# Optimization experiments

Measured on AMD Instinct MI355X. Metric: run time of the kernel, lower is better.

Reference implementation:

```python
import jax, jax.numpy as jnp
import numpy as np

NUM_HEADS = 8
LN_EPS = 1e-5


def setup_inputs() -> dict:
    key = jax.random.key(0)
    k1, k2, k3 = jax.random.split(key, 3)
    B, N, C = 1, 4096, 256
    before = jax.random.normal(k1, (B, N, C), dtype=jnp.float32)
    after = jax.random.normal(k2, (B, N, C), dtype=jnp.float32)
    W_qkv = jax.random.normal(k3, (3 * C, C), dtype=jnp.float32) * (C ** -0.5)
    d = C // NUM_HEADS
    gamma = jnp.ones((d,), dtype=jnp.float32)
    beta = jnp.zeros((d,), dtype=jnp.float32)
    return {"before": before, "after": after, "W_qkv": W_qkv, "gamma": gamma, "beta": beta}


def _qkv_norm(x, W_qkv, gamma, beta, H):
    # x: [B,N,C] -> q,k,v each [B,H,N,d], LayerNorm over d applied to all of qkv
    B, N, C = x.shape
    d = C // H
    t = jnp.einsum('bnc,oc->bno', x, W_qkv)            # [B,N,3C]
    t = t.reshape(B, N, 3, H, d).transpose(2, 0, 3, 1, 4)  # [3,B,H,N,d]
    mu = jnp.mean(t, axis=-1, keepdims=True)
    var = jnp.mean(jnp.square(t - mu), axis=-1, keepdims=True)
    t = (t - mu) * jax.lax.rsqrt(var + LN_EPS) * gamma + beta
    return t[0], t[1], t[2]


def _cross_attn(q, k, v, scale):
    # q,k,v: [B,H,N,d] -> context [B,N,C]
    attn = jax.nn.softmax(jnp.einsum('bhqd,bhkd->bhqk', q, k) * scale, axis=-1)
    ctx = jnp.einsum('bhqk,bhkd->bhqd', attn, v)
    B, H, N, d = ctx.shape
    return ctx.transpose(0, 2, 1, 3).reshape(B, N, H * d)


def reference(before, after, W_qkv, gamma, beta):
    H = NUM_HEADS
    C = before.shape[-1]
    d = C // H
    scale = d ** -0.5
    q_b, k_b, v_b = _qkv_norm(before, W_qkv, gamma, beta, H)
    q_a, k_a, v_a = _qkv_norm(after, W_qkv, gamma, beta, H)
    context_a = _cross_attn(q_b, k_a, v_a, scale)  # before attends to after
    context_b = _cross_attn(q_a, k_b, v_b, scale)  # after attends to before
    return (context_b, context_a)
```

## Files before the change

### kernel.cpp

```cpp
#include <hip/hip_runtime.h>


typedef __attribute__((ext_vector_type(8))) short short8;
typedef __attribute__((ext_vector_type(4))) float float4v;
typedef __attribute__((ext_vector_type(4))) unsigned int uint4v;

#define NTOK 4096
#define CDIM 256
#define HEADS 8
#define DHEAD 32

#define QOFF 0
#define KOFF (2*HEADS*NTOK*DHEAD)
#define VOFF (2*(2*HEADS*NTOK*DHEAD))
#define WOFF (3*(2*HEADS*NTOK*DHEAD))

__device__ inline unsigned short f2bf(float f) {
    union { float f; unsigned u; } v; v.f = f;
    unsigned r = v.u + 0x7FFFu + ((v.u >> 16) & 1u);
    return (unsigned short)(r >> 16);
}

__global__ __launch_bounds__(256) void wconv_kernel(
    const float* __restrict__ W, unsigned short* __restrict__ ws)
{
    int idx = blockIdx.x*256 + threadIdx.x;
    int R = idx >> 5, oct = idx & 31;
    int C = oct * 8;
    const float4* p = reinterpret_cast<const float4*>(W + R*CDIM + C);
    float4 a = p[0], b = p[1];
    short8 f;
    f[0]=(short)f2bf(a.x); f[1]=(short)f2bf(a.y); f[2]=(short)f2bf(a.z); f[3]=(short)f2bf(a.w);
    f[4]=(short)f2bf(b.x); f[5]=(short)f2bf(b.y); f[6]=(short)f2bf(b.z); f[7]=(short)f2bf(b.w);
    int o32 = R >> 5, r = R & 31;
    int kk = C >> 5, quad = (C >> 3) & 3;
    int dst = o32*8192 + (kk*2 + (r>>4))*512 + (quad*16 + (r&15))*8;
    *reinterpret_cast<short8*>(ws + WOFF + dst) = f;
}

__global__ __launch_bounds__(256) void qkv_ln_kernel(
    const float* __restrict__ before, const float* __restrict__ after,
    const float* __restrict__ gamma, const float* __restrict__ beta,
    unsigned short* __restrict__ ws)
{
    const int tid  = threadIdx.x;
    const int lane = tid & 63;
    const int w    = tid >> 6;
    const int quad = lane >> 4;
    const int l16  = lane & 15;
    const int rt   = blockIdx.x >> 3;
    const int oq   = blockIdx.x & 7;

    const int mrow_frag = rt*64 + w*16 + l16;
    const int inp_f = mrow_frag >> 12;
    const int n_f   = mrow_frag & 4095;
    const float* x = inp_f ? after : before;

    short8 afrag[8];
#pragma unroll
    for (int kk = 0; kk < 8; kk++) {
        const float4* p = reinterpret_cast<const float4*>(x + n_f*CDIM + kk*32 + quad*8);
        float4 a = p[0], b = p[1];
        short8 f;
        f[0]=(short)f2bf(a.x); f[1]=(short)f2bf(a.y); f[2]=(short)f2bf(a.z); f[3]=(short)f2bf(a.w);
        f[4]=(short)f2bf(b.x); f[5]=(short)f2bf(b.y); f[6]=(short)f2bf(b.z); f[7]=(short)f2bf(b.w);
        afrag[kk] = f;
    }

    const float g0  = gamma[l16], g1  = gamma[16+l16];
    const float be0 = beta[l16],  be1 = beta[16+l16];
    const float cscale = 0.17677669529663687f * 1.4426950408889634f;

    const int mrow_out  = rt*64 + w*16 + quad*4;
    const int inp_o     = mrow_out >> 12;
    const int n_o_base  = mrow_out & 4095;

    const unsigned short* wbf = ws + WOFF;

    for (int o32 = oq*3; o32 < oq*3 + 3; o32++) {
        const unsigned short* wb = wbf + o32*8192 + lane*8;
        float4v acc0 = {0.f,0.f,0.f,0.f}, acc1 = {0.f,0.f,0.f,0.f};
#pragma unroll
        for (int kk = 0; kk < 8; kk++) {
            short8 b0 = *reinterpret_cast<const short8*>(wb + (kk*2    )*512);
            short8 b1 = *reinterpret_cast<const short8*>(wb + (kk*2 + 1)*512);
            acc0 = __builtin_amdgcn_mfma_f32_16x16x32_bf16(afrag[kk], b0, acc0, 0,0,0);
            acc1 = __builtin_amdgcn_mfma_f32_16x16x32_bf16(afrag[kk], b1, acc1, 0,0,0);
        }

        const int which = o32 >> 3;
        const int h     = o32 & 7;
        unsigned short* qk = ws + (which == 0 ? QOFF : KOFF) + ((inp_o*HEADS + h)*NTOK)*DHEAD;
        unsigned short* vt = ws + VOFF + ((inp_o*HEADS + h)*DHEAD)*NTOK;
        const float qs = (which == 0) ? cscale : 1.0f;

#pragma unroll
        for (int i = 0; i < 4; i++) {
            float sum = acc0[i] + acc1[i];
            float sq  = acc0[i]*acc0[i] + acc1[i]*acc1[i];
#pragma unroll
            for (int m = 1; m < 16; m <<= 1) {
                sum += __shfl_xor(sum, m);
                sq  += __shfl_xor(sq,  m);
            }
            float mu   = sum * (1.0f/32.0f);
            float var  = sq * (1.0f/32.0f) - mu*mu;
            float rstd = rsqrtf(var + 1e-5f);
            float v0 = ((acc0[i]-mu)*rstd*g0 + be0) * qs;
            float v1 = ((acc1[i]-mu)*rstd*g1 + be1) * qs;
            int n = n_o_base + i;
            if (which < 2) {
                qk[n*DHEAD + l16]      = f2bf(v0);
                qk[n*DHEAD + 16 + l16] = f2bf(v1);
            } else {
                int kb = n >> 5, ki = n & 31;
                int slot = ((ki & 15) >> 2)*8 + (ki & 3) + ((ki >> 4) << 2);
                int kp2 = kb*32 + slot;
                vt[l16*NTOK + kp2]       = f2bf(v0);
                vt[(16+l16)*NTOK + kp2]  = f2bf(v1);
            }
        }
    }
}

__global__ __launch_bounds__(256, 4) void attn_kernel(
    const unsigned short* __restrict__ ws, float* __restrict__ out)
{
    __shared__ unsigned short vlds[2][32*136];

    const int b    = blockIdx.x;
    const int xcd  = b & 7;
    const int i_   = b >> 3;
    const int combo = xcd*2 + (i_ >> 6);
    const int h  = combo & 7;
    const int X  = combo >> 3;
    const int qb = i_ & 63;

    const int qinp = 1 - X, kvinp = X;
    const int tid  = threadIdx.x;
    const int lane = tid & 63;
    const int w    = tid >> 6;
    const int qh   = w & 1;
    const int kh   = w >> 1;
    const int quad = lane >> 4;
    const int l16  = lane & 15;

    const unsigned short* qbase = ws + QOFF + ((qinp*HEADS + h)*NTOK)*DHEAD;
    const unsigned short* kbase = ws + KOFF + ((kvinp*HEADS + h)*NTOK)*DHEAD;
    const unsigned short* vbase = ws + VOFF + ((kvinp*HEADS + h)*DHEAD)*NTOK;

    const int q0 = qb*64 + qh*32;
    const short8 qf0 = *reinterpret_cast<const short8*>(qbase + (q0 + l16)*DHEAD      + quad*8);
    const short8 qf1 = *reinterpret_cast<const short8*>(qbase + (q0 + 16 + l16)*DHEAD + quad*8);

    const unsigned short* kp   = kbase + (kh*2048 + l16)*DHEAD + quad*8;
    const unsigned short* vsrc = vbase + kh*2048;

    const short8 ones = {0x3F80,0x3F80,0x3F80,0x3F80,0x3F80,0x3F80,0x3F80,0x3F80};

    float4v O00 = {0,0,0,0}, O01 = {0,0,0,0}, O10 = {0,0,0,0}, O11 = {0,0,0,0};
    float4v L0  = {0,0,0,0}, L1  = {0,0,0,0};

    unsigned short* vh = vlds[kh];
    const int t2 = qh*64 + lane;

    for (int j = 0; j < 16; j++) {
        __syncthreads();
#pragma unroll
        for (int r = 0; r < 4; r++) {
            int c = t2 + 128*r;
            short8 d = *reinterpret_cast<const short8*>(vsrc + (c>>4)*NTOK + j*128 + (c&15)*8);
            *reinterpret_cast<short8*>(vh + (c>>4)*136 + (c&15)*8) = d;
        }
        __syncthreads();

#pragma unroll
        for (int grp = 0; grp < 4; grp++) {
            short8 kf0 = *reinterpret_cast<const short8*>(kp + (j*128 + grp*32     )*DHEAD);
            short8 kf1 = *reinterpret_cast<const short8*>(kp + (j*128 + grp*32 + 16)*DHEAD);
            short8 v0  = *reinterpret_cast<const short8*>(vh + l16*136      + grp*32 + quad*8);
            short8 v1  = *reinterpret_cast<const short8*>(vh + (16+l16)*136 + grp*32 + quad*8);
#pragma unroll
            for (int s = 0; s < 2; s++) {
                const short8 qf = s ? qf1 : qf0;
                float4v z = {0,0,0,0};
                float4v S0 = __builtin_amdgcn_mfma_f32_16x16x32_bf16(kf0, qf, z, 0,0,0);
                float4v S1 = __builtin_amdgcn_mfma_f32_16x16x32_bf16(kf1, qf, z, 0,0,0);
                union { float f; unsigned u; } u0,u1,u2,u3,u4,u5,u6,u7;
                u0.f = __builtin_amdgcn_exp2f(S0[0]);
                u1.f = __builtin_amdgcn_exp2f(S0[1]);
                u2.f = __builtin_amdgcn_exp2f(S0[2]);
                u3.f = __builtin_amdgcn_exp2f(S0[3]);
                u4.f = __builtin_amdgcn_exp2f(S1[0]);
                u5.f = __builtin_amdgcn_exp2f(S1[1]);
                u6.f = __builtin_amdgcn_exp2f(S1[2]);
                u7.f = __builtin_amdgcn_exp2f(S1[3]);
                union { short8 s8; uint4v u4v; } pf;
                pf.u4v[0] = __builtin_amdgcn_perm(u1.u, u0.u, 0x07060302u);
                pf.u4v[1] = __builtin_amdgcn_perm(u3.u, u2.u, 0x07060302u);
                pf.u4v[2] = __builtin_amdgcn_perm(u5.u, u4.u, 0x07060302u);
                pf.u4v[3] = __builtin_amdgcn_perm(u7.u, u6.u, 0x07060302u);
                if (s == 0) {
                    O00 = __builtin_amdgcn_mfma_f32_16x16x32_bf16(pf.s8, v0,   O00, 0,0,0);
                    O01 = __builtin_amdgcn_mfma_f32_16x16x32_bf16(pf.s8, v1,   O01, 0,0,0);
                    L0  = __builtin_amdgcn_mfma_f32_16x16x32_bf16(pf.s8, ones, L0,  0,0,0);
                } else {
                    O10 = __builtin_amdgcn_mfma_f32_16x16x32_bf16(pf.s8, v0,   O10, 0,0,0);
                    O11 = __builtin_amdgcn_mfma_f32_16x16x32_bf16(pf.s8, v1,   O11, 0,0,0);
                    L1  = __builtin_amdgcn_mfma_f32_16x16x32_bf16(pf.s8, ones, L1,  0,0,0);
                }
            }
        }
    }

    __syncthreads();

    float* comb = reinterpret_cast<float*>(&vlds[0][0]) + qh*(32*34);
    if (kh == 1) {
#pragma unroll
        for (int s = 0; s < 2; s++)
#pragma unroll
            for (int i = 0; i < 4; i++) {
                int row = s*16 + quad*4 + i;
                comb[row*34 + l16]      = (s ? O10[i] : O00[i]);
                comb[row*34 + 16 + l16] = (s ? O11[i] : O01[i]);
                if (l16 == 0) comb[row*34 + 32] = (s ? L1[i] : L0[i]);
            }
    }
    __syncthreads();

    if (kh == 0) {
        float* ob = out + (size_t)X*NTOK*CDIM + h*DHEAD;
#pragma unroll
        for (int s = 0; s < 2; s++) {
#pragma unroll
            for (int i = 0; i < 4; i++) {
                int row = s*16 + quad*4 + i;
                float l = (s ? L1[i] : L0[i]) + comb[row*34 + 32];
                float inv = 1.0f / l;
                float a = ((s ? O10[i] : O00[i]) + comb[row*34 + l16])      * inv;
                float b = ((s ? O11[i] : O01[i]) + comb[row*34 + 16 + l16]) * inv;
                int orow = q0 + row;
                ob[orow*CDIM + l16]      = a;
                ob[orow*CDIM + 16 + l16] = b;
            }
        }
    }
}

extern "C" void kernel_launch(void* const* d_in, const int* in_sizes, int n_in,
                              void* d_out, int out_size, void* d_ws, size_t ws_size,
                              hipStream_t stream)
{
    const float* before = (const float*)d_in[0];
    const float* after  = (const float*)d_in[1];
    const float* W      = (const float*)d_in[2];
    const float* gamma  = (const float*)d_in[3];
    const float* beta   = (const float*)d_in[4];
    float* out          = (float*)d_out;
    unsigned short* ws  = (unsigned short*)d_ws;

    hipLaunchKernelGGL(wconv_kernel, dim3(96), dim3(256), 0, stream, W, ws);
    hipLaunchKernelGGL(qkv_ln_kernel, dim3(1024), dim3(256), 0, stream,
                       before, after, gamma, beta, ws);
    hipLaunchKernelGGL(attn_kernel, dim3(1024), dim3(256), 0, stream, ws, out);
}
```

Before: 146.5 us.

## Double-buffer V tiles in LDS with register prefetch and hoist K loads

V tiles now go through two LDS buffers. The next tile's global loads are issued into registers before the current tile's MFMA work and written to the other buffer afterwards, so one barrier per iteration replaces two. All four groups of K fragments are also loaded up front to overlap their latency with compute. This doubles the LDS footprint, which may lower occupancy, and the extra prefetch and K registers add register pressure.

Result: no change. 145.1 us (-0.9%).

```diff
diff --git a/kernel.cpp b/kernel.cpp
--- a/kernel.cpp
+++ b/kernel.cpp
@@ -126,7 +126,7 @@
 __global__ __launch_bounds__(256, 4) void attn_kernel(
     const unsigned short* __restrict__ ws, float* __restrict__ out)
 {
-    __shared__ unsigned short vlds[2][32*136];
+    __shared__ unsigned short vlds[2][2][32*136];
 
     const int b    = blockIdx.x;
     const int xcd  = b & 7;
@@ -161,31 +161,49 @@
     float4v O00 = {0,0,0,0}, O01 = {0,0,0,0}, O10 = {0,0,0,0}, O11 = {0,0,0,0};
     float4v L0  = {0,0,0,0}, L1  = {0,0,0,0};
 
-    unsigned short* vh = vlds[kh];
     const int t2 = qh*64 + lane;
+    const int vr = t2 >> 4;
+    const int vc = (t2 & 15)*8;
+
+    {
+        short8 vreg[4];
+#pragma unroll
+        for (int r = 0; r < 4; r++)
+            vreg[r] = *reinterpret_cast<const short8*>(vsrc + (vr + 8*r)*NTOK + vc);
+#pragma unroll
+        for (int r = 0; r < 4; r++)
+            *reinterpret_cast<short8*>(&vlds[kh][0][(vr + 8*r)*136 + vc]) = vreg[r];
+    }
 
     for (int j = 0; j < 16; j++) {
         __syncthreads();
-#pragma unroll
-        for (int r = 0; r < 4; r++) {
-            int c = t2 + 128*r;
-            short8 d = *reinterpret_cast<const short8*>(vsrc + (c>>4)*NTOK + j*128 + (c&15)*8);
-            *reinterpret_cast<short8*>(vh + (c>>4)*136 + (c&15)*8) = d;
-        }
-        __syncthreads();
-
+        const unsigned short* vh = vlds[kh][j&1];
+
+        short8 vreg[4];
+        const bool pf = (j + 1 < 16);
+        if (pf) {
+#pragma unroll
+            for (int r = 0; r < 4; r++)
+                vreg[r] = *reinterpret_cast<const short8*>(vsrc + (vr + 8*r)*NTOK + (j+1)*128 + vc);
+        }
+
+        short8 kf0[4], kf1[4];
 #pragma unroll
         for (int grp = 0; grp < 4; grp++) {
-            short8 kf0 = *reinterpret_cast<const short8*>(kp + (j*128 + grp*32     )*DHEAD);
-            short8 kf1 = *reinterpret_cast<const short8*>(kp + (j*128 + grp*32 + 16)*DHEAD);
-            short8 v0  = *reinterpret_cast<const short8*>(vh + l16*136      + grp*32 + quad*8);
-            short8 v1  = *reinterpret_cast<const short8*>(vh + (16+l16)*136 + grp*32 + quad*8);
+            kf0[grp] = *reinterpret_cast<const short8*>(kp + (j*128 + grp*32     )*DHEAD);
+            kf1[grp] = *reinterpret_cast<const short8*>(kp + (j*128 + grp*32 + 16)*DHEAD);
+        }
+
+#pragma unroll
+        for (int grp = 0; grp < 4; grp++) {
+            short8 v0 = *reinterpret_cast<const short8*>(vh + l16*136      + grp*32 + quad*8);
+            short8 v1 = *reinterpret_cast<const short8*>(vh + (16+l16)*136 + grp*32 + quad*8);
 #pragma unroll
             for (int s = 0; s < 2; s++) {
                 const short8 qf = s ? qf1 : qf0;
                 float4v z = {0,0,0,0};
-                float4v S0 = __builtin_amdgcn_mfma_f32_16x16x32_bf16(kf0, qf, z, 0,0,0);
-                float4v S1 = __builtin_amdgcn_mfma_f32_16x16x32_bf16(kf1, qf, z, 0,0,0);
+                float4v S0 = __builtin_amdgcn_mfma_f32_16x16x32_bf16(kf0[grp], qf, z, 0,0,0);
+                float4v S1 = __builtin_amdgcn_mfma_f32_16x16x32_bf16(kf1[grp], qf, z, 0,0,0);
                 union { float f; unsigned u; } u0,u1,u2,u3,u4,u5,u6,u7;
                 u0.f = __builtin_amdgcn_exp2f(S0[0]);
                 u1.f = __builtin_amdgcn_exp2f(S0[1]);
@@ -195,27 +213,33 @@
                 u5.f = __builtin_amdgcn_exp2f(S1[1]);
                 u6.f = __builtin_amdgcn_exp2f(S1[2]);
                 u7.f = __builtin_amdgcn_exp2f(S1[3]);
-                union { short8 s8; uint4v u4v; } pf;
-                pf.u4v[0] = __builtin_amdgcn_perm(u1.u, u0.u, 0x07060302u);
-                pf.u4v[1] = __builtin_amdgcn_perm(u3.u, u2.u, 0x07060302u);
-                pf.u4v[2] = __builtin_amdgcn_perm(u5.u, u4.u, 0x07060302u);
-                pf.u4v[3] = __builtin_amdgcn_perm(u7.u, u6.u, 0x07060302u);
+                union { short8 s8; uint4v u4v; } pfr;
+                pfr.u4v[0] = __builtin_amdgcn_perm(u1.u, u0.u, 0x07060302u);
+                pfr.u4v[1] = __builtin_amdgcn_perm(u3.u, u2.u, 0x07060302u);
+                pfr.u4v[2] = __builtin_amdgcn_perm(u5.u, u4.u, 0x07060302u);
+                pfr.u4v[3] = __builtin_amdgcn_perm(u7.u, u6.u, 0x07060302u);
                 if (s == 0) {
-                    O00 = __builtin_amdgcn_mfma_f32_16x16x32_bf16(pf.s8, v0,   O00, 0,0,0);
-                    O01 = __builtin_amdgcn_mfma_f32_16x16x32_bf16(pf.s8, v1,   O01, 0,0,0);
-                    L0  = __builtin_amdgcn_mfma_f32_16x16x32_bf16(pf.s8, ones, L0,  0,0,0);
+                    O00 = __builtin_amdgcn_mfma_f32_16x16x32_bf16(pfr.s8, v0,   O00, 0,0,0);
+                    O01 = __builtin_amdgcn_mfma_f32_16x16x32_bf16(pfr.s8, v1,   O01, 0,0,0);
+                    L0  = __builtin_amdgcn_mfma_f32_16x16x32_bf16(pfr.s8, ones, L0,  0,0,0);
                 } else {
-                    O10 = __builtin_amdgcn_mfma_f32_16x16x32_bf16(pf.s8, v0,   O10, 0,0,0);
-                    O11 = __builtin_amdgcn_mfma_f32_16x16x32_bf16(pf.s8, v1,   O11, 0,0,0);
-                    L1  = __builtin_amdgcn_mfma_f32_16x16x32_bf16(pf.s8, ones, L1,  0,0,0);
+                    O10 = __builtin_amdgcn_mfma_f32_16x16x32_bf16(pfr.s8, v0,   O10, 0,0,0);
+                    O11 = __builtin_amdgcn_mfma_f32_16x16x32_bf16(pfr.s8, v1,   O11, 0,0,0);
+                    L1  = __builtin_amdgcn_mfma_f32_16x16x32_bf16(pfr.s8, ones, L1,  0,0,0);
                 }
             }
         }
+
+        if (pf) {
+#pragma unroll
+            for (int r = 0; r < 4; r++)
+                *reinterpret_cast<short8*>(&vlds[kh][(j+1)&1][(vr + 8*r)*136 + vc]) = vreg[r];
+        }
     }
 
     __syncthreads();
 
-    float* comb = reinterpret_cast<float*>(&vlds[0][0]) + qh*(32*34);
+    float* comb = reinterpret_cast<float*>(&vlds[0][0][0]) + qh*(32*34);
     if (kh == 1) {
 #pragma unroll
         for (int s = 0; s < 2; s++)
```

## Split attention key range across two blocks with atomic accumulation and normalize pass

Applied to the files above, without the earlier changes.

Doubles the attention grid so each block handles half of the keys (a split-K style scheme). Partial unnormalized outputs and row sums are accumulated with atomicAdd into the zeroed output and a workspace buffer, and a new kernel then divides by the row sum. The aim is more parallelism and occupancy, at the cost of two memsets, float atomics, an extra launch and a full extra pass over the output. Softmax still has no max subtraction, as before.

Result: slower. 155.4 us (+6.1%).

```diff
diff --git a/kernel.cpp b/kernel.cpp
--- a/kernel.cpp
+++ b/kernel.cpp
@@ -14,6 +14,7 @@
 #define KOFF (2*HEADS*NTOK*DHEAD)
 #define VOFF (2*(2*HEADS*NTOK*DHEAD))
 #define WOFF (3*(2*HEADS*NTOK*DHEAD))
+#define LOFF (WOFF + 24*8192)
 
 __device__ inline unsigned short f2bf(float f) {
     union { float f; unsigned u; } v; v.f = f;
@@ -131,17 +132,18 @@
     const int b    = blockIdx.x;
     const int xcd  = b & 7;
     const int i_   = b >> 3;
-    const int combo = xcd*2 + (i_ >> 6);
-    const int h  = combo & 7;
-    const int X  = combo >> 3;
-    const int qb = i_ & 63;
+    const int combo = xcd*2 + (i_ >> 7);
+    const int h   = combo & 7;
+    const int X   = combo >> 3;
+    const int qb  = (i_ >> 1) & 63;
+    const int khо = i_ & 1;
 
     const int qinp = 1 - X, kvinp = X;
     const int tid  = threadIdx.x;
     const int lane = tid & 63;
     const int w    = tid >> 6;
     const int qh   = w & 1;
-    const int kh   = w >> 1;
+    const int khi  = w >> 1;
     const int quad = lane >> 4;
     const int l16  = lane & 15;
 
@@ -150,27 +152,29 @@
     const unsigned short* vbase = ws + VOFF + ((kvinp*HEADS + h)*DHEAD)*NTOK;
 
     const int q0 = qb*64 + qh*32;
+    const int k0 = khо*2048 + khi*1024;
     const short8 qf0 = *reinterpret_cast<const short8*>(qbase + (q0 + l16)*DHEAD      + quad*8);
     const short8 qf1 = *reinterpret_cast<const short8*>(qbase + (q0 + 16 + l16)*DHEAD + quad*8);
 
-    const unsigned short* kp   = kbase + (kh*2048 + l16)*DHEAD + quad*8;
-    const unsigned short* vsrc = vbase + kh*2048;
+    const unsigned short* kp   = kbase + (k0 + l16)*DHEAD + quad*8;
+    const unsigned short* vsrc = vbase + k0;
 
     const short8 ones = {0x3F80,0x3F80,0x3F80,0x3F80,0x3F80,0x3F80,0x3F80,0x3F80};
 
     float4v O00 = {0,0,0,0}, O01 = {0,0,0,0}, O10 = {0,0,0,0}, O11 = {0,0,0,0};
     float4v L0  = {0,0,0,0}, L1  = {0,0,0,0};
 
-    unsigned short* vh = vlds[kh];
+    unsigned short* vh = vlds[khi];
     const int t2 = qh*64 + lane;
-
-    for (int j = 0; j < 16; j++) {
+    const int vr = t2 >> 4;
+    const int vc = (t2 & 15)*8;
+
+    for (int j = 0; j < 8; j++) {
         __syncthreads();
 #pragma unroll
         for (int r = 0; r < 4; r++) {
-            int c = t2 + 128*r;
-            short8 d = *reinterpret_cast<const short8*>(vsrc + (c>>4)*NTOK + j*128 + (c&15)*8);
-            *reinterpret_cast<short8*>(vh + (c>>4)*136 + (c&15)*8) = d;
+            short8 d = *reinterpret_cast<const short8*>(vsrc + (vr + 8*r)*NTOK + j*128 + vc);
+            *reinterpret_cast<short8*>(vh + (vr + 8*r)*136 + vc) = d;
         }
         __syncthreads();
 
@@ -195,19 +199,19 @@
                 u5.f = __builtin_amdgcn_exp2f(S1[1]);
                 u6.f = __builtin_amdgcn_exp2f(S1[2]);
                 u7.f = __builtin_amdgcn_exp2f(S1[3]);
-                union { short8 s8; uint4v u4v; } pf;
-                pf.u4v[0] = __builtin_amdgcn_perm(u1.u, u0.u, 0x07060302u);
-                pf.u4v[1] = __builtin_amdgcn_perm(u3.u, u2.u, 0x07060302u);
-                pf.u4v[2] = __builtin_amdgcn_perm(u5.u, u4.u, 0x07060302u);
-                pf.u4v[3] = __builtin_amdgcn_perm(u7.u, u6.u, 0x07060302u);
+                union { short8 s8; uint4v u4v; } pfr;
+                pfr.u4v[0] = __builtin_amdgcn_perm(u1.u, u0.u, 0x07060302u);
+                pfr.u4v[1] = __builtin_amdgcn_perm(u3.u, u2.u, 0x07060302u);
+                pfr.u4v[2] = __builtin_amdgcn_perm(u5.u, u4.u, 0x07060302u);
+                pfr.u4v[3] = __builtin_amdgcn_perm(u7.u, u6.u, 0x07060302u);
                 if (s == 0) {
-                    O00 = __builtin_amdgcn_mfma_f32_16x16x32_bf16(pf.s8, v0,   O00, 0,0,0);
-                    O01 = __builtin_amdgcn_mfma_f32_16x16x32_bf16(pf.s8, v1,   O01, 0,0,0);
-                    L0  = __builtin_amdgcn_mfma_f32_16x16x32_bf16(pf.s8, ones, L0,  0,0,0);
+                    O00 = __builtin_amdgcn_mfma_f32_16x16x32_bf16(pfr.s8, v0,   O00, 0,0,0);
+                    O01 = __builtin_amdgcn_mfma_f32_16x16x32_bf16(pfr.s8, v1,   O01, 0,0,0);
+                    L0  = __builtin_amdgcn_mfma_f32_16x16x32_bf16(pfr.s8, ones, L0,  0,0,0);
                 } else {
-                    O10 = __builtin_amdgcn_mfma_f32_16x16x32_bf16(pf.s8, v0,   O10, 0,0,0);
-                    O11 = __builtin_amdgcn_mfma_f32_16x16x32_bf16(pf.s8, v1,   O11, 0,0,0);
-                    L1  = __builtin_amdgcn_mfma_f32_16x16x32_bf16(pf.s8, ones, L1,  0,0,0);
+                    O10 = __builtin_amdgcn_mfma_f32_16x16x32_bf16(pfr.s8, v0,   O10, 0,0,0);
+                    O11 = __builtin_amdgcn_mfma_f32_16x16x32_bf16(pfr.s8, v1,   O11, 0,0,0);
+                    L1  = __builtin_amdgcn_mfma_f32_16x16x32_bf16(pfr.s8, ones, L1,  0,0,0);
                 }
             }
         }
@@ -216,7 +220,7 @@
     __syncthreads();
 
     float* comb = reinterpret_cast<float*>(&vlds[0][0]) + qh*(32*34);
-    if (kh == 1) {
+    if (khi == 1) {
 #pragma unroll
         for (int s = 0; s < 2; s++)
 #pragma unroll
@@ -229,23 +233,42 @@
     }
     __syncthreads();
 
-    if (kh == 0) {
+    if (khi == 0) {
         float* ob = out + (size_t)X*NTOK*CDIM + h*DHEAD;
+        float* lp = reinterpret_cast<float*>(const_cast<unsigned short*>(ws) + LOFF)
+                    + (X*HEADS + h)*NTOK;
 #pragma unroll
         for (int s = 0; s < 2; s++) {
 #pragma unroll
             for (int i = 0; i < 4; i++) {
                 int row = s*16 + quad*4 + i;
                 float l = (s ? L1[i] : L0[i]) + comb[row*34 + 32];
-                float inv = 1.0f / l;
-                float a = ((s ? O10[i] : O00[i]) + comb[row*34 + l16])      * inv;
-                float b = ((s ? O11[i] : O01[i]) + comb[row*34 + 16 + l16]) * inv;
+                float a = (s ? O10[i] : O00[i]) + comb[row*34 + l16];
+                float bb = (s ? O11[i] : O01[i]) + comb[row*34 + 16 + l16];
                 int orow = q0 + row;
-                ob[orow*CDIM + l16]      = a;
-                ob[orow*CDIM + 16 + l16] = b;
-            }
-        }
-    }
+                atomicAdd(&ob[orow*CDIM + l16],      a);
+                atomicAdd(&ob[orow*CDIM + 16 + l16], bb);
+                if (l16 == 0) atomicAdd(&lp[orow], l);
+            }
+        }
+    }
+}
+
+__global__ __launch_bounds__(256) void norm_kernel(
+    float* __restrict__ out, const unsigned short* __restrict__ ws)
+{
+    const float* l = reinterpret_cast<const float*>(ws + LOFF);
+    int idx = blockIdx.x*256 + threadIdx.x;
+    int o = idx * 4;
+    int c = o & 255;
+    int n = (o >> 8) & 4095;
+    int X = o >> 20;
+    float lv = l[(X*HEADS + (c >> 5))*NTOK + n];
+    float inv = 1.0f / lv;
+    float4* p = reinterpret_cast<float4*>(out) + idx;
+    float4 v = *p;
+    v.x *= inv; v.y *= inv; v.z *= inv; v.w *= inv;
+    *p = v;
 }
 
 extern "C" void kernel_launch(void* const* d_in, const int* in_sizes, int n_in,
@@ -260,8 +283,12 @@
     float* out          = (float*)d_out;
     unsigned short* ws  = (unsigned short*)d_ws;
 
+    hipMemsetAsync(d_out, 0, (size_t)out_size * sizeof(float), stream);
+    hipMemsetAsync(ws + LOFF, 0, (size_t)2*HEADS*NTOK*sizeof(float), stream);
+
     hipLaunchKernelGGL(wconv_kernel, dim3(96), dim3(256), 0, stream, W, ws);
     hipLaunchKernelGGL(qkv_ln_kernel, dim3(1024), dim3(256), 0, stream,
                        before, after, gamma, beta, ws);
-    hipLaunchKernelGGL(attn_kernel, dim3(1024), dim3(256), 0, stream, ws, out);
-}
+    hipLaunchKernelGGL(attn_kernel, dim3(2048), dim3(256), 0, stream, ws, out);
+    hipLaunchKernelGGL(norm_kernel, dim3(2048), dim3(256), 0, stream, out, ws);
+}
```
